# Optimization experiments

Measured on AMD Instinct MI355X. Metric: run time of the kernel, lower is better.

## Reference

```python
import jax, jax.numpy as jnp
import numpy as np

STRIDES = [1, 2, 4, 8]
K = 512  # num_nodes_per_scale
HID = 128
OUT = 128


def conv1x1(x, w, b):
    # x: [B,C,H,W], w: [O,C], b: [O]
    return jnp.einsum('bchw,oc->bohw', x, w) + b[None, :, None, None]


def head(x, w1, b1, w2, b2):
    # Conv1x1 -> exact GELU -> Conv1x1 (matches nn.GELU default)
    return conv1x1(jax.nn.gelu(conv1x1(x, w1, b1), approximate=False), w2, b2)


def max_pool(x, r):
    # torch max_pool2d(kernel=2r+1, stride=1, padding=r) pads with -inf
    k = 2 * r + 1
    return jax.lax.reduce_window(x, -jnp.inf, jax.lax.max,
                                 (1, 1, k, k), (1, 1, 1, 1),
                                 [(0, 0), (0, 0), (r, r), (r, r)])


def simple_nms(w, r):
    ninf = jnp.asarray(-jnp.inf, w.dtype)
    max_mask = w == max_pool(w, r)
    for _ in range(2):
        supp_mask = max_pool(max_mask.astype(w.dtype), r) > 0
        supp_w = jnp.where(supp_mask, ninf, w)
        new_max = supp_w == max_pool(supp_w, r)
        max_mask = max_mask | (new_max & ~supp_mask)
    return jnp.where(max_mask, w, ninf)


def bilinear_sample(feat, gx, gy):
    # grid_sample(mode='bilinear', align_corners=False, padding_mode='zeros')
    # feat: [B,C,H,W]; gx,gy: [B,K] normalized coords in [-1,1]
    B, C, H, W = feat.shape
    ix = ((gx + 1.0) * W - 1.0) * 0.5
    iy = ((gy + 1.0) * H - 1.0) * 0.5
    x0 = jnp.floor(ix); y0 = jnp.floor(iy)
    x1 = x0 + 1.0;      y1 = y0 + 1.0
    wx1 = ix - x0;      wy1 = iy - y0
    flat = feat.reshape(B, C, H * W)

    def gather(xc, yc):
        valid = (xc >= 0) & (xc <= W - 1) & (yc >= 0) & (yc <= H - 1)
        xi = jnp.clip(xc, 0, W - 1).astype(jnp.int32)
        yi = jnp.clip(yc, 0, H - 1).astype(jnp.int32)
        lin = yi * W + xi  # [B,K]
        g = jnp.take_along_axis(flat, lin[:, None, :], axis=2)  # [B,C,K]
        return g * valid[:, None, :].astype(feat.dtype)

    v00 = gather(x0, y0); v01 = gather(x1, y0)
    v10 = gather(x0, y1); v11 = gather(x1, y1)
    out = (v00 * ((1 - wx1) * (1 - wy1))[:, None, :]
           + v01 * (wx1 * (1 - wy1))[:, None, :]
           + v10 * ((1 - wx1) * wy1)[:, None, :]
           + v11 * (wx1 * wy1)[:, None, :])
    return out.transpose(0, 2, 1)  # [B,K,C]


def process_scale(fm, rw1, rb1, rw2, rb2, fw1, fb1, fw2, fb2):
    B, C, H, W = fm.shape
    rel = head(fm, rw1, rb1, rw2, rb2)   # [B,1,H,W]
    proj = head(fm, fw1, fb1, fw2, fb2)  # [B,OUT,H,W]
    border = max(1, H // 64)
    r = max(1, H // 64)
    m = jnp.zeros((H, W), bool).at[border:H - border, border:W - border].set(True)
    rel = jnp.where(m[None, None], rel, -jnp.inf)
    rel = simple_nms(rel, r)
    vals, idx = jax.lax.top_k(rel.reshape(B, H * W), K)  # [B,K]
    y = idx // W
    x = idx % W
    nx = x.astype(jnp.float32) / (W - 1) * 2.0 - 1.0
    ny = y.astype(jnp.float32) / (H - 1) * 2.0 - 1.0
    feats = bilinear_sample(proj, nx, ny)  # [B,K,OUT]
    return jnp.stack([nx, ny], axis=-1), vals, feats


def setup_inputs() -> dict:
    key = jax.random.key(0)
    ks = jax.random.split(key, 12)
    B = 2
    inp = {
        'fm1': jax.random.normal(ks[0], (B, HID, 512, 512), jnp.float32),
        'fm2': jax.random.normal(ks[1], (B, HID, 256, 256), jnp.float32),
        'fm4': jax.random.normal(ks[2], (B, HID, 128, 128), jnp.float32),
        'fm8': jax.random.normal(ks[3], (B, HID, 64, 64), jnp.float32),
        'rw1': jax.random.normal(ks[4], (OUT, HID), jnp.float32) * 0.05,
        'rb1': jnp.zeros((OUT,), jnp.float32),
        'rw2': jax.random.normal(ks[5], (1, OUT), jnp.float32) * 0.05,
        'rb2': jnp.zeros((1,), jnp.float32),
        'fw1': jax.random.normal(ks[6], (OUT, HID), jnp.float32) * 0.05,
        'fb1': jnp.zeros((OUT,), jnp.float32),
        'fw2': jax.random.normal(ks[7], (OUT, OUT), jnp.float32) * 0.05,
        'fb2': jnp.zeros((OUT,), jnp.float32),
    }
    return inp


def reference(fm1, fm2, fm4, fm8, rw1, rb1, rw2, rb2, fw1, fb1, fw2, fb2):
    outs = [process_scale(fm, rw1, rb1, rw2, rb2, fw1, fb1, fw2, fb2)
            for fm in (fm1, fm2, fm4, fm8)]
    all_norm_xy = jnp.concatenate([o[0] for o in outs], axis=1)      # [B,4K,2]
    all_reliability = jnp.concatenate([o[1] for o in outs], axis=1)  # [B,4K]
    all_features = jnp.concatenate([o[2] for o in outs], axis=1)     # [B,4K,OUT]
    return all_norm_xy, all_reliability, all_features
```

## Files before the change

kernel.cpp:

```cpp
#include <hip/hip_runtime.h>
#include <math.h>

#define CH 128
#define KSEL 512
#define CAP 4096
#define TOT 2048
#define TS 32
#define NEG_INF (-__builtin_inff())

typedef short s8v __attribute__((ext_vector_type(8)));
typedef float f4v __attribute__((ext_vector_type(4)));

__device__ __forceinline__ float gelu_exact(float v) {
    return v * 0.5f * (1.0f + erff(v * 0.70710678118654752440f));
}

__device__ __forceinline__ void split3(float v, unsigned short& h,
                                       unsigned short& m, unsigned short& l)
{
    union { float f; unsigned u; } a; a.f = v;
    unsigned rh = a.u + 0x7FFFu + ((a.u >> 16) & 1u);
    h = (unsigned short)(rh >> 16);
    union { unsigned u; float f; } fh; fh.u = rh & 0xFFFF0000u;
    float r1 = v - fh.f;
    union { float f; unsigned u; } bu; bu.f = r1;
    unsigned rm = bu.u + 0x7FFFu + ((bu.u >> 16) & 1u);
    m = (unsigned short)(rm >> 16);
    union { unsigned u; float f; } fm2; fm2.u = rm & 0xFFFF0000u;
    float r2 = r1 - fm2.f;
    union { float f; unsigned u; } cu; cu.f = r2;
    unsigned rl = cu.u + 0x7FFFu + ((cu.u >> 16) & 1u);
    l = (unsigned short)(rl >> 16);
}

__global__ __launch_bounds__(256) void wconv_kernel(const float* __restrict__ w1,
                                                    unsigned short* __restrict__ wfrag)
{
    for (int e = blockIdx.x * 256 + threadIdx.x; e < 49152; e += gridDim.x * 256) {
        int fid = e >> 9;
        int r = e & 511;
        int lane = r >> 3;
        int el = r & 7;
        int plane = fid % 3;
        int fq = fid / 3;
        int kc = fq >> 3, ot = fq & 7;
        int och = ot * 16 + (lane & 15);
        int k = kc * 32 + ((lane >> 4) << 3) + el;
        unsigned short h, m, l;
        split3(w1[och * CH + k], h, m, l);
        wfrag[e] = (plane == 0) ? h : (plane == 1) ? m : l;
    }
}

__global__ __launch_bounds__(1024) void rel_mfma_kernel(
    const float* __restrict__ fm0, const float* __restrict__ fm1,
    const float* __restrict__ fm2, const float* __restrict__ fm3,
    const unsigned short* __restrict__ wfrag,
    const float* __restrict__ b1, const float* __restrict__ w2,
    const float* __restrict__ b2, float* __restrict__ rel)
{
    __shared__ uint4 WfQ[6144];
    __shared__ float w2s[128], b1s[128];
    unsigned short* Wf = (unsigned short*)WfQ;

    const int tid = threadIdx.x;
    {
        const uint4* src = (const uint4*)wfrag;
        for (int i = tid; i < 6144; i += 1024) WfQ[i] = src[i];
    }
    if (tid < 128) { w2s[tid] = w2[tid]; b1s[tid] = b1[tid]; }
    __syncthreads();

    const float* fms[4] = {fm0, fm1, fm2, fm3};
    const int pre1 = 2048, pre2 = 2560, pre3 = 2688;
    const int relo[4] = {0, 524288, 655360, 688128};
    const float b2v = b2[0];

    const int lane = tid & 63;
    const int j = lane & 15;
    const int g8 = (lane >> 4) << 3;
    const int w = tid >> 6;

    for (int T = blockIdx.x; T < 2720; T += gridDim.x) {
        int s = (T >= pre1) + (T >= pre2) + (T >= pre3);
        int t2 = T - ((s == 0) ? 0 : (s == 1) ? pre1 : (s == 2) ? pre2 : pre3);
        int Wd = 512 >> s, HW = Wd * Wd;
        int p0 = t2 * 256;
        int b = (p0 >= HW) ? 1 : 0;
        int pb = p0 - b * HW;
        int pw = pb + w * 16;
        const float* fp = fms[s] + (size_t)b * CH * HW;
        int rr = Wd >> 6; if (rr < 1) rr = 1;

        const float* pxp = fp + pw + j;

        f4v acc[8];
        #pragma unroll
        for (int ot = 0; ot < 8; ++ot) {
            acc[ot][0] = 0.f; acc[ot][1] = 0.f; acc[ot][2] = 0.f; acc[ot][3] = 0.f;
        }

        #pragma unroll 1
        for (int kc = 0; kc < 4; ++kc) {
            float xv[8];
            #pragma unroll
            for (int e = 0; e < 8; ++e)
                xv[e] = pxp[(size_t)(kc * 32 + g8 + e) * HW];

            s8v bh, bm, bl;
            #pragma unroll
            for (int e = 0; e < 8; ++e) {
                unsigned short h, m, l;
                split3(xv[e], h, m, l);
                bh[e] = (short)h; bm[e] = (short)m; bl[e] = (short)l;
            }
            #pragma unroll
            for (int ot = 0; ot < 8; ++ot) {
                const unsigned short* fb = Wf + (((kc << 3) + ot) * 3) * 512 + (lane << 3);
                s8v ah = *(const s8v*)fb;
                s8v am = *(const s8v*)(fb + 512);
                s8v al = *(const s8v*)(fb + 1024);
                acc[ot] = __builtin_amdgcn_mfma_f32_16x16x32_bf16(ah, bh, acc[ot], 0, 0, 0);
                acc[ot] = __builtin_amdgcn_mfma_f32_16x16x32_bf16(ah, bm, acc[ot], 0, 0, 0);
                acc[ot] = __builtin_amdgcn_mfma_f32_16x16x32_bf16(am, bh, acc[ot], 0, 0, 0);
                acc[ot] = __builtin_amdgcn_mfma_f32_16x16x32_bf16(am, bm, acc[ot], 0, 0, 0);
                acc[ot] = __builtin_amdgcn_mfma_f32_16x16x32_bf16(ah, bl, acc[ot], 0, 0, 0);
                acc[ot] = __builtin_amdgcn_mfma_f32_16x16x32_bf16(al, bh, acc[ot], 0, 0, 0);
            }
        }

        float part = 0.f;
        #pragma unroll
        for (int ot = 0; ot < 8; ++ot) {
            #pragma unroll
            for (int r = 0; r < 4; ++r) {
                int och = ot * 16 + ((lane >> 4) << 2) + r;
                part += w2s[och] * gelu_exact(acc[ot][r] + b1s[och]);
            }
        }
        part += __shfl_xor(part, 16);
        part += __shfl_xor(part, 32);
        if (lane < 16) {
            int p = pw + lane;
            int y = p / Wd, x = p - y * Wd;
            bool inte = (y >= rr) && (y < Wd - rr) && (x >= rr) && (x < Wd - rr);
            rel[relo[s] + b * HW + p] = inte ? (part + b2v) : NEG_INF;
        }
    }
}

__device__ __forceinline__ void nms_decode(int blk, int& s, int& b, int& ty, int& tx,
                                           int& Wd, int& HW, int& r, int& ro)
{
    s = (blk >= 512) + (blk >= 640) + (blk >= 672);
    int t2 = blk - ((s == 0) ? 0 : (s == 1) ? 512 : (s == 2) ? 640 : 672);
    Wd = 512 >> s; HW = Wd * Wd;
    int tpb = (Wd / TS) * (Wd / TS);
    b = t2 / tpb;
    int t = t2 - b * tpb;
    ty = t / (Wd / TS); tx = t - ty * (Wd / TS);
    r = Wd >> 6; if (r < 1) r = 1;
    ro = (s == 0) ? 0 : (s == 1) ? 524288 : (s == 2) ? 655360 : 688128;
}

__global__ __launch_bounds__(256) void nms_init_all(
    const float* __restrict__ rel, float* __restrict__ mask)
{
    int s, b, ty, tx, W, HW, r, ro;
    nms_decode(blockIdx.x, s, b, ty, tx, W, HW, r, ro);
    int H = W;
    int L = TS + 2 * r;
    __shared__ float wtile[48][49];
    __shared__ float t1[48][49];
    const float* wp = rel + ro + (size_t)b * HW;
    for (int idx = threadIdx.x; idx < L * L; idx += 256) {
        int i = idx / L, j = idx - i * L;
        int gy = min(max(ty * TS - r + i, 0), H - 1);
        int gx = min(max(tx * TS - r + j, 0), W - 1);
        wtile[i][j] = wp[gy * W + gx];
    }
    __syncthreads();
    for (int idx = threadIdx.x; idx < L * TS; idx += 256) {
        int i = idx / TS, j = idx - i * TS;
        float m = wtile[i][j];
        for (int d = 1; d <= 2 * r; ++d) m = fmaxf(m, wtile[i][j + d]);
        t1[i][j] = m;
    }
    __syncthreads();
    for (int idx = threadIdx.x; idx < TS * TS; idx += 256) {
        int i = idx / TS, j = idx - i * TS;
        float m = t1[i][j];
        for (int d = 1; d <= 2 * r; ++d) m = fmaxf(m, t1[i + d][j]);
        mask[ro + (size_t)b * HW + (ty * TS + i) * W + (tx * TS + j)] =
            (wtile[i + r][j + r] == m) ? 1.0f : 0.0f;
    }
}

__global__ __launch_bounds__(256) void nms_fused_all(
    const float* __restrict__ rel, float* __restrict__ mask, int do_compact,
    float* __restrict__ lval, int* __restrict__ lidx, int* __restrict__ counts)
{
    int s, b, ty, tx, W, HW, r, ro;
    nms_decode(blockIdx.x, s, b, ty, tx, W, HW, r, ro);
    int H = W;
    int L = TS + 4 * r;
    int gy0 = ty * TS - 2 * r, gx0 = tx * TS - 2 * r;
    __shared__ float A[64][65], B[64][65], C[64][65];
    const float* mp = mask + ro + (size_t)b * HW;
    const float* rp = rel + ro + (size_t)b * HW;

    for (int idx = threadIdx.x; idx < L * L; idx += 256) {
        int i = idx / L, j = idx - i * L;
        int gy = min(max(gy0 + i, 0), H - 1);
        int gx = min(max(gx0 + j, 0), W - 1);
        A[i][j] = mp[gy * W + gx];
    }
    __syncthreads();
    int w1c = L - 2 * r;
    for (int idx = threadIdx.x; idx < L * w1c; idx += 256) {
        int i = idx / w1c, j = idx - i * w1c + r;
        float m = A[i][j - r];
        for (int d = 1; d <= 2 * r; ++d) m = fmaxf(m, A[i][j - r + d]);
        B[i][j] = m;
    }
    __syncthreads();
    for (int idx = threadIdx.x; idx < w1c * w1c; idx += 256) {
        int i = idx / w1c + r, j = idx % w1c + r;
        float m = B[i - r][j];
        for (int d = 1; d <= 2 * r; ++d) m = fmaxf(m, B[i - r + d][j]);
        C[i][j] = m;
    }
    float mreg[4];
    #pragma unroll
    for (int k = 0; k < 4; ++k) {
        int idx = threadIdx.x + k * 256;
        int i = idx >> 5, j = idx & 31;
        mreg[k] = A[2 * r + i][2 * r + j];
    }
    __syncthreads();
    for (int idx = threadIdx.x; idx < w1c * w1c; idx += 256) {
        int i = idx / w1c + r, j = idx % w1c + r;
        int gy = min(max(gy0 + i, 0), H - 1);
        int gx = min(max(gx0 + j, 0), W - 1);
        B[i][j] = (C[i][j] > 0.f) ? NEG_INF : rp[gy * W + gx];
    }
    __syncthreads();
    for (int idx = threadIdx.x; idx < w1c * TS; idx += 256) {
        int i = idx / TS + r, j = idx % TS + 2 * r;
        float m = B[i][j - r];
        for (int d = 1; d <= 2 * r; ++d) m = fmaxf(m, B[i][j - r + d]);
        A[i][j] = m;
    }
    __syncthreads();
    #pragma unroll
    for (int k = 0; k < 4; ++k) {
        int idx = threadIdx.x + k * 256;
        int i = idx >> 5, j = idx & 31;
        int ci = 2 * r + i, cj = 2 * r + j;
        float m = A[ci - r][cj];
        for (int d = 1; d <= 2 * r; ++d) m = fmaxf(m, A[ci - r + d][cj]);
        bool supp = C[ci][cj] > 0.f;
        bool newm = (B[ci][cj] == m) && !supp;
        bool fin = (mreg[k] > 0.f) || newm;
        int gy = ty * TS + i, gx = tx * TS + j;
        size_t g = ro + (size_t)b * HW + gy * W + gx;
        if (!do_compact) {
            mask[g] = fin ? 1.f : 0.f;
        } else if (fin) {
            float v = rp[gy * W + gx];
            if (!isinf(v)) {
                int bs = b * 4 + s;
                int slot = atomicAdd(&counts[bs], 1);
                if (slot < CAP) { lval[bs * CAP + slot] = v; lidx[bs * CAP + slot] = gy * W + gx; }
            }
        }
    }
}

__global__ __launch_bounds__(1024) void sort_topk_kernel(
    const float* __restrict__ lval, const int* __restrict__ lidx,
    const int* __restrict__ counts, float* __restrict__ tv, int* __restrict__ ti)
{
    __shared__ float sv[CAP];
    __shared__ int   si[CAP];
    int bs = blockIdx.x;
    int M = counts[bs]; if (M > CAP) M = CAP;
    for (int i = threadIdx.x; i < CAP; i += 1024) {
        if (i < M) { sv[i] = lval[bs * CAP + i]; si[i] = lidx[bs * CAP + i]; }
        else       { sv[i] = NEG_INF;            si[i] = 0x7FFFFFFF; }
    }
    __syncthreads();
    for (int k = 2; k <= CAP; k <<= 1) {
        for (int j = k >> 1; j > 0; j >>= 1) {
            for (int t = threadIdx.x; t < CAP; t += 1024) {
                int p = t ^ j;
                if (p > t) {
                    float va = sv[t], vb = sv[p];
                    int   ia = si[t], ib = si[p];
                    bool aBefore = (va > vb) || (va == vb && ia < ib);
                    bool up = ((t & k) == 0);
                    if (up ? !aBefore : aBefore) {
                        sv[t] = vb; sv[p] = va; si[t] = ib; si[p] = ia;
                    }
                }
            }
            __syncthreads();
        }
    }
    for (int j = threadIdx.x; j < KSEL; j += 1024) {
        if (j < M) { tv[bs * KSEL + j] = sv[j]; ti[bs * KSEL + j] = si[j]; }
        else       { tv[bs * KSEL + j] = NEG_INF; ti[bs * KSEL + j] = j - M; }
    }
}

__global__ __launch_bounds__(256) void coords_kernel(
    const float* __restrict__ tv, const int* __restrict__ ti, float* __restrict__ out)
{
    int gid = blockIdx.x * blockDim.x + threadIdx.x;
    if (gid >= 8 * KSEL) return;
    int bs = gid / KSEL, k = gid - bs * KSEL;
    int b = bs >> 2, s = bs & 3;
    int W = 512 >> s;
    int idx = ti[gid];
    int y = idx / W, x = idx - y * W;
    float nx = (float)x / (float)(W - 1) * 2.0f - 1.0f;
    float ny = (float)y / (float)(W - 1) * 2.0f - 1.0f;
    int pos = s * KSEL + k;
    out[((size_t)b * TOT + pos) * 2 + 0] = nx;
    out[((size_t)b * TOT + pos) * 2 + 1] = ny;
    out[2 * TOT * 2 + (size_t)b * TOT + pos] = tv[gid];
}

__global__ __launch_bounds__(128) void feats_kernel(
    const float* __restrict__ fm0, const float* __restrict__ fm1,
    const float* __restrict__ fm2, const float* __restrict__ fm3,
    const float* __restrict__ w1, const float* __restrict__ b1,
    const float* __restrict__ w2, const float* __restrict__ b2,
    const int* __restrict__ ti, float* __restrict__ out)
{
    int blk = blockIdx.x;
    int bs = blk / KSEL, k = blk - bs * KSEL;
    int b = bs >> 2, s = bs & 3;
    int W = 512 >> s, H = W, HW = H * W;
    const float* fm = (s == 0) ? fm0 : (s == 1) ? fm1 : (s == 2) ? fm2 : fm3;

    int idx = ti[bs * KSEL + k];
    int yi0 = idx / W, xi0 = idx - yi0 * W;
    float nx = (float)xi0 / (float)(W - 1) * 2.0f - 1.0f;
    float ny = (float)yi0 / (float)(H - 1) * 2.0f - 1.0f;
    float ix = ((nx + 1.0f) * (float)W - 1.0f) * 0.5f;
    float iy = ((ny + 1.0f) * (float)H - 1.0f) * 0.5f;
    float x0 = floorf(ix), y0 = floorf(iy);
    float x1 = x0 + 1.0f,  y1 = y0 + 1.0f;
    float wx1 = ix - x0, wy1 = iy - y0;

    float xs[4]  = {x0, x1, x0, x1};
    float ysv[4] = {y0, y0, y1, y1};
    float wn[4]  = {(1.0f - wx1) * (1.0f - wy1), wx1 * (1.0f - wy1),
                    (1.0f - wx1) * wy1,          wx1 * wy1};
    int pix[4]; float wv[4];
    #pragma unroll
    for (int n = 0; n < 4; ++n) {
        bool valid = (xs[n] >= 0.0f) && (xs[n] <= (float)(W - 1)) &&
                     (ysv[n] >= 0.0f) && (ysv[n] <= (float)(H - 1));
        int xc = (int)fminf(fmaxf(xs[n], 0.0f), (float)(W - 1));
        int yc = (int)fminf(fmaxf(ysv[n], 0.0f), (float)(H - 1));
        pix[n] = yc * W + xc;
        wv[n] = valid ? wn[n] : 0.0f;
    }

    __shared__ float xls[4][CH];
    __shared__ float hmix[CH];
    int o = threadIdx.x;
    {
        const float* fb_ = fm + ((size_t)b * CH + o) * HW;
        #pragma unroll
        for (int n = 0; n < 4; ++n) xls[n][o] = fb_[pix[n]];
    }
    __syncthreads();

    float h0 = b1[o], h1 = h0, h2 = h0, h3 = h0;
    const float* wr = w1 + o * CH;
    for (int c = 0; c < CH; ++c) {
        float w = wr[c];
        h0 = fmaf(w, xls[0][c], h0);
        h1 = fmaf(w, xls[1][c], h1);
        h2 = fmaf(w, xls[2][c], h2);
        h3 = fmaf(w, xls[3][c], h3);
    }
    float wsum = wv[0] + wv[1] + wv[2] + wv[3];
    hmix[o] = wv[0] * gelu_exact(h0) + wv[1] * gelu_exact(h1) +
              wv[2] * gelu_exact(h2) + wv[3] * gelu_exact(h3);
    __syncthreads();

    float acc = b2[o] * wsum;
    const float* w2r = w2 + o * CH;
    for (int c = 0; c < CH; ++c) acc = fmaf(w2r[c], hmix[c], acc);
    out[2 * TOT * 2 + 2 * TOT + ((size_t)b * TOT + s * KSEL + k) * CH + o] = acc;
}

extern "C" void kernel_launch(void* const* d_in, const int* in_sizes, int n_in,
                              void* d_out, int out_size, void* d_ws, size_t ws_size,
                              hipStream_t stream)
{
    const float* fm[4] = {(const float*)d_in[0], (const float*)d_in[1],
                          (const float*)d_in[2], (const float*)d_in[3]};
    const float* rw1 = (const float*)d_in[4];
    const float* rb1 = (const float*)d_in[5];
    const float* rw2 = (const float*)d_in[6];
    const float* rb2 = (const float*)d_in[7];
    const float* fw1 = (const float*)d_in[8];
    const float* fb1 = (const float*)d_in[9];
    const float* fw2 = (const float*)d_in[10];
    const float* fb2 = (const float*)d_in[11];

    float* ws = (float*)d_ws;
    float* rel   = ws;
    float* mask  = ws + 696320;
    float* lval  = ws + 1392640;
    int*   lidx  = (int*)(ws + 1425408);
    int*   counts= (int*)(ws + 1458176);
    float* tv    = ws + 1458184;
    int*   ti    = (int*)(ws + 1462280);
    unsigned short* wfrag = (unsigned short*)(ws + 1466376);

    hipMemsetAsync(counts, 0, 8 * sizeof(int), stream);
    wconv_kernel<<<64, 256, 0, stream>>>(rw1, wfrag);
    rel_mfma_kernel<<<256, 1024, 0, stream>>>(fm[0], fm[1], fm[2], fm[3],
                                              wfrag, rb1, rw2, rb2, rel);

    nms_init_all<<<680, 256, 0, stream>>>(rel, mask);
    nms_fused_all<<<680, 256, 0, stream>>>(rel, mask, 0, lval, lidx, counts);
    nms_fused_all<<<680, 256, 0, stream>>>(rel, mask, 1, lval, lidx, counts);

    sort_topk_kernel<<<8, 1024, 0, stream>>>(lval, lidx, counts, tv, ti);
    coords_kernel<<<16, 256, 0, stream>>>(tv, ti, (float*)d_out);
    feats_kernel<<<4096, 128, 0, stream>>>(fm[0], fm[1], fm[2], fm[3],
                                           fw1, fb1, fw2, fb2, ti, (float*)d_out);
}
```

Baseline: 547.2 us.

## Restructure reliability conv to 32x32 MFMA with register-resident weight fragments per wave

The reliability head's 1x1 conv now gives each block 32 pixels, and each of its 4 waves owns 32 output channels. Each wave keeps its weight fragments (hi/mid/lo bf16 splits) in registers for the whole kernel, so the large LDS weight copy and the per-tile LDS weight reads are gone. It uses 32x32x16 bf16 MFMAs and reduces the per-wave partial dot products through LDS, and split3 now uses the HIP bf16 intrinsics. The costs are many more, smaller tiles and two block barriers per tile. Each thread also holds 24 vector registers of weights, which may raise register pressure, and every wave reloads the same pixel data from global memory.

```diff
diff --git a/kernel.cpp b/kernel.cpp
--- a/kernel.cpp
+++ b/kernel.cpp
@@ -1,4 +1,5 @@
 #include <hip/hip_runtime.h>
+#include <hip/hip_bf16.h>
 #include <math.h>
 
 #define CH 128
@@ -9,7 +10,7 @@
 #define NEG_INF (-__builtin_inff())
 
 typedef short s8v __attribute__((ext_vector_type(8)));
-typedef float f4v __attribute__((ext_vector_type(4)));
+typedef float f16v __attribute__((ext_vector_type(16)));
 
 __device__ __forceinline__ float gelu_exact(float v) {
     return v * 0.5f * (1.0f + erff(v * 0.70710678118654752440f));
@@ -18,94 +19,98 @@
 __device__ __forceinline__ void split3(float v, unsigned short& h,
                                        unsigned short& m, unsigned short& l)
 {
-    union { float f; unsigned u; } a; a.f = v;
-    unsigned rh = a.u + 0x7FFFu + ((a.u >> 16) & 1u);
-    h = (unsigned short)(rh >> 16);
-    union { unsigned u; float f; } fh; fh.u = rh & 0xFFFF0000u;
-    float r1 = v - fh.f;
-    union { float f; unsigned u; } bu; bu.f = r1;
-    unsigned rm = bu.u + 0x7FFFu + ((bu.u >> 16) & 1u);
-    m = (unsigned short)(rm >> 16);
-    union { unsigned u; float f; } fm2; fm2.u = rm & 0xFFFF0000u;
-    float r2 = r1 - fm2.f;
-    union { float f; unsigned u; } cu; cu.f = r2;
-    unsigned rl = cu.u + 0x7FFFu + ((cu.u >> 16) & 1u);
-    l = (unsigned short)(rl >> 16);
+    union BU { __hip_bfloat16 b; unsigned short u; };
+    __hip_bfloat16 hb = __float2bfloat16(v);
+    BU x; x.b = hb; h = x.u;
+    float r1 = v - __bfloat162float(hb);
+    __hip_bfloat16 mb = __float2bfloat16(r1);
+    BU y; y.b = mb; m = y.u;
+    float r2 = r1 - __bfloat162float(mb);
+    __hip_bfloat16 lb = __float2bfloat16(r2);
+    BU z; z.b = lb; l = z.u;
 }
 
 __global__ __launch_bounds__(256) void wconv_kernel(const float* __restrict__ w1,
                                                     unsigned short* __restrict__ wfrag)
 {
-    for (int e = blockIdx.x * 256 + threadIdx.x; e < 49152; e += gridDim.x * 256) {
-        int fid = e >> 9;
-        int r = e & 511;
+    for (int ei = blockIdx.x * 256 + threadIdx.x; ei < 49152; ei += gridDim.x * 256) {
+        int f = ei >> 9;
+        int r = ei & 511;
         int lane = r >> 3;
-        int el = r & 7;
-        int plane = fid % 3;
-        int fq = fid / 3;
-        int kc = fq >> 3, ot = fq & 7;
-        int och = ot * 16 + (lane & 15);
-        int k = kc * 32 + ((lane >> 4) << 3) + el;
+        int e = r & 7;
+        int plane = f % 3;
+        int fq = f / 3;
+        int g = fq >> 3, kc = fq & 7;
+        int och = g * 32 + (lane & 31);
+        int k = kc * 16 + ((lane >> 5) << 3) + e;
         unsigned short h, m, l;
         split3(w1[och * CH + k], h, m, l);
-        wfrag[e] = (plane == 0) ? h : (plane == 1) ? m : l;
-    }
-}
-
-__global__ __launch_bounds__(1024) void rel_mfma_kernel(
+        wfrag[ei] = (plane == 0) ? h : (plane == 1) ? m : l;
+    }
+}
+
+__global__ __launch_bounds__(256) void rel_mfma_kernel(
     const float* __restrict__ fm0, const float* __restrict__ fm1,
     const float* __restrict__ fm2, const float* __restrict__ fm3,
     const unsigned short* __restrict__ wfrag,
     const float* __restrict__ b1, const float* __restrict__ w2,
     const float* __restrict__ b2, float* __restrict__ rel)
 {
-    __shared__ uint4 WfQ[6144];
     __shared__ float w2s[128], b1s[128];
-    unsigned short* Wf = (unsigned short*)WfQ;
+    __shared__ float partLds[4][32];
 
     const int tid = threadIdx.x;
-    {
-        const uint4* src = (const uint4*)wfrag;
-        for (int i = tid; i < 6144; i += 1024) WfQ[i] = src[i];
-    }
+    const int lane = tid & 63;
+    const int w = tid >> 6;
     if (tid < 128) { w2s[tid] = w2[tid]; b1s[tid] = b1[tid]; }
     __syncthreads();
 
+    #define WLD(KC, PL) (*(const s8v*)(wfrag + (((w * 8 + (KC)) * 3 + (PL)) << 9) + (lane << 3)))
+    s8v a0h = WLD(0,0), a0m = WLD(0,1), a0l = WLD(0,2);
+    s8v a1h = WLD(1,0), a1m = WLD(1,1), a1l = WLD(1,2);
+    s8v a2h = WLD(2,0), a2m = WLD(2,1), a2l = WLD(2,2);
+    s8v a3h = WLD(3,0), a3m = WLD(3,1), a3l = WLD(3,2);
+    s8v a4h = WLD(4,0), a4m = WLD(4,1), a4l = WLD(4,2);
+    s8v a5h = WLD(5,0), a5m = WLD(5,1), a5l = WLD(5,2);
+    s8v a6h = WLD(6,0), a6m = WLD(6,1), a6l = WLD(6,2);
+    s8v a7h = WLD(7,0), a7m = WLD(7,1), a7l = WLD(7,2);
+    #undef WLD
+
     const float* fms[4] = {fm0, fm1, fm2, fm3};
-    const int pre1 = 2048, pre2 = 2560, pre3 = 2688;
+    const int pre1 = 16384, pre2 = 20480, pre3 = 21504;
     const int relo[4] = {0, 524288, 655360, 688128};
     const float b2v = b2[0];
-
-    const int lane = tid & 63;
-    const int j = lane & 15;
-    const int g8 = (lane >> 4) << 3;
-    const int w = tid >> 6;
-
-    for (int T = blockIdx.x; T < 2720; T += gridDim.x) {
+    const int px = lane & 31;
+    const int kb = (lane >> 5) << 3;
+
+    for (int T = blockIdx.x; T < 21760; T += gridDim.x) {
         int s = (T >= pre1) + (T >= pre2) + (T >= pre3);
         int t2 = T - ((s == 0) ? 0 : (s == 1) ? pre1 : (s == 2) ? pre2 : pre3);
         int Wd = 512 >> s, HW = Wd * Wd;
-        int p0 = t2 * 256;
+        int p0 = t2 * 32;
         int b = (p0 >= HW) ? 1 : 0;
         int pb = p0 - b * HW;
-        int pw = pb + w * 16;
-        const float* fp = fms[s] + (size_t)b * CH * HW;
+        const float* xp = fms[s] + (size_t)b * CH * HW + pb + px;
         int rr = Wd >> 6; if (rr < 1) rr = 1;
 
-        const float* pxp = fp + pw + j;
-
-        f4v acc[8];
+        f16v acc;
         #pragma unroll
-        for (int ot = 0; ot < 8; ++ot) {
-            acc[ot][0] = 0.f; acc[ot][1] = 0.f; acc[ot][2] = 0.f; acc[ot][3] = 0.f;
-        }
+        for (int q = 0; q < 16; ++q) acc[q] = 0.f;
+
+        #define MFMA6(AH, AM, AL)                                                   \
+            acc = __builtin_amdgcn_mfma_f32_32x32x16_bf16(AH, bh, acc, 0, 0, 0);    \
+            acc = __builtin_amdgcn_mfma_f32_32x32x16_bf16(AH, bm, acc, 0, 0, 0);    \
+            acc = __builtin_amdgcn_mfma_f32_32x32x16_bf16(AM, bh, acc, 0, 0, 0);    \
+            acc = __builtin_amdgcn_mfma_f32_32x32x16_bf16(AM, bm, acc, 0, 0, 0);    \
+            acc = __builtin_amdgcn_mfma_f32_32x32x16_bf16(AH, bl, acc, 0, 0, 0);    \
+            acc = __builtin_amdgcn_mfma_f32_32x32x16_bf16(AL, bh, acc, 0, 0, 0);
 
         #pragma unroll 1
-        for (int kc = 0; kc < 4; ++kc) {
+        for (int kc = 0; kc < 8; ++kc) {
             float xv[8];
             #pragma unroll
             for (int e = 0; e < 8; ++e)
-                xv[e] = pxp[(size_t)(kc * 32 + g8 + e) * HW];
+                xv[e] = xp[(size_t)(kc * 16 + kb + e) * HW];
 
             s8v bh, bm, bl;
             #pragma unroll
@@ -114,38 +119,38 @@
                 split3(xv[e], h, m, l);
                 bh[e] = (short)h; bm[e] = (short)m; bl[e] = (short)l;
             }
-            #pragma unroll
-            for (int ot = 0; ot < 8; ++ot) {
-                const unsigned short* fb = Wf + (((kc << 3) + ot) * 3) * 512 + (lane << 3);
-                s8v ah = *(const s8v*)fb;
-                s8v am = *(const s8v*)(fb + 512);
-                s8v al = *(const s8v*)(fb + 1024);
-                acc[ot] = __builtin_amdgcn_mfma_f32_16x16x32_bf16(ah, bh, acc[ot], 0, 0, 0);
-                acc[ot] = __builtin_amdgcn_mfma_f32_16x16x32_bf16(ah, bm, acc[ot], 0, 0, 0);
-                acc[ot] = __builtin_amdgcn_mfma_f32_16x16x32_bf16(am, bh, acc[ot], 0, 0, 0);
-                acc[ot] = __builtin_amdgcn_mfma_f32_16x16x32_bf16(am, bm, acc[ot], 0, 0, 0);
-                acc[ot] = __builtin_amdgcn_mfma_f32_16x16x32_bf16(ah, bl, acc[ot], 0, 0, 0);
-                acc[ot] = __builtin_amdgcn_mfma_f32_16x16x32_bf16(al, bh, acc[ot], 0, 0, 0);
+            switch (kc) {
+                case 0: MFMA6(a0h, a0m, a0l) break;
+                case 1: MFMA6(a1h, a1m, a1l) break;
+                case 2: MFMA6(a2h, a2m, a2l) break;
+                case 3: MFMA6(a3h, a3m, a3l) break;
+                case 4: MFMA6(a4h, a4m, a4l) break;
+                case 5: MFMA6(a5h, a5m, a5l) break;
+                case 6: MFMA6(a6h, a6m, a6l) break;
+                default: MFMA6(a7h, a7m, a7l) break;
             }
         }
+        #undef MFMA6
 
         float part = 0.f;
         #pragma unroll
-        for (int ot = 0; ot < 8; ++ot) {
-            #pragma unroll
-            for (int r = 0; r < 4; ++r) {
-                int och = ot * 16 + ((lane >> 4) << 2) + r;
-                part += w2s[och] * gelu_exact(acc[ot][r] + b1s[och]);
-            }
+        for (int q = 0; q < 16; ++q) {
+            int row = (q & 3) + ((q >> 2) << 3) + ((lane >> 5) << 2);
+            int och = w * 32 + row;
+            part += w2s[och] * gelu_exact(acc[q] + b1s[och]);
         }
-        part += __shfl_xor(part, 16);
         part += __shfl_xor(part, 32);
-        if (lane < 16) {
-            int p = pw + lane;
+        if (lane < 32) partLds[w][lane] = part;
+        __syncthreads();
+        if (tid < 32) {
+            float tot = partLds[0][tid] + partLds[1][tid] +
+                        partLds[2][tid] + partLds[3][tid] + b2v;
+            int p = pb + tid;
             int y = p / Wd, x = p - y * Wd;
             bool inte = (y >= rr) && (y < Wd - rr) && (x >= rr) && (x < Wd - rr);
-            rel[relo[s] + b * HW + p] = inte ? (part + b2v) : NEG_INF;
+            rel[relo[s] + b * HW + p] = inte ? tot : NEG_INF;
         }
+        __syncthreads();
     }
 }
 
@@ -426,8 +431,8 @@
 
     hipMemsetAsync(counts, 0, 8 * sizeof(int), stream);
     wconv_kernel<<<64, 256, 0, stream>>>(rw1, wfrag);
-    rel_mfma_kernel<<<256, 1024, 0, stream>>>(fm[0], fm[1], fm[2], fm[3],
-                                              wfrag, rb1, rw2, rb2, rel);
+    rel_mfma_kernel<<<768, 256, 0, stream>>>(fm[0], fm[1], fm[2], fm[3],
+                                             wfrag, rb1, rw2, rb2, rel);
 
     nms_init_all<<<680, 256, 0, stream>>>(rel, mask);
     nms_fused_all<<<680, 256, 0, stream>>>(rel, mask, 0, lval, lidx, counts);
```

Result: slower. 785.7 us (+43.6%).
